# Kernel tuning notes

Measured on AMD Instinct MI355X. Metric: run time of the kernel, lower is better.

The kernel has to match this reference:

```python
import jax, jax.numpy as jnp
import numpy as np

N_TOTAL = 2_000_000   # total particles across all events
N_EVENTS = 20_000     # number of events (segments)
H = 64                # phi/rho hidden width
OUT = 10              # output classes


def _lin(x, W, b):
    # torch nn.Linear: y = x @ W.T + b
    return x @ W.T + b


def setup_inputs() -> dict:
    key = jax.random.key(0)
    ks = jax.random.split(key, 24)
    s = 0.1  # small init scale
    inp = {
        "values": jax.random.normal(ks[0], (N_TOTAL,), dtype=jnp.float32),
        "seg_ids": jnp.sort(jax.random.randint(ks[1], (N_TOTAL,), 0, N_EVENTS)),
        "p1w0": jax.random.normal(ks[2], (H, 1), dtype=jnp.float32) * s,
        "p1b0": jax.random.normal(ks[3], (H,), dtype=jnp.float32) * s,
        "p1w1": jax.random.normal(ks[4], (H, H), dtype=jnp.float32) * s,
        "p1b1": jax.random.normal(ks[5], (H,), dtype=jnp.float32) * s,
        "r1w0": jax.random.normal(ks[6], (H, H), dtype=jnp.float32) * s,
        "r1b0": jax.random.normal(ks[7], (H,), dtype=jnp.float32) * s,
        "r1w1": jax.random.normal(ks[8], (H, H), dtype=jnp.float32) * s,
        "r1b1": jax.random.normal(ks[9], (H,), dtype=jnp.float32) * s,
        "o1w": jax.random.normal(ks[10], (H, H), dtype=jnp.float32) * s,
        "o1b": jax.random.normal(ks[11], (H,), dtype=jnp.float32) * s,
        "p2w0": jax.random.normal(ks[12], (H, H), dtype=jnp.float32) * s,
        "p2b0": jax.random.normal(ks[13], (H,), dtype=jnp.float32) * s,
        "p2w1": jax.random.normal(ks[14], (H, H), dtype=jnp.float32) * s,
        "p2b1": jax.random.normal(ks[15], (H,), dtype=jnp.float32) * s,
        "r2w0": jax.random.normal(ks[16], (H, H), dtype=jnp.float32) * s,
        "r2b0": jax.random.normal(ks[17], (H,), dtype=jnp.float32) * s,
        "r2w1": jax.random.normal(ks[18], (H, H), dtype=jnp.float32) * s,
        "r2b1": jax.random.normal(ks[19], (H,), dtype=jnp.float32) * s,
        "o2w": jax.random.normal(ks[20], (OUT, H), dtype=jnp.float32) * s,
        "o2b": jax.random.normal(ks[21], (OUT,), dtype=jnp.float32) * s,
    }
    return inp


def reference(values, seg_ids, p1w0, p1b0, p1w1, p1b1, r1w0, r1b0, r1w1, r1b1,
              o1w, o1b, p2w0, p2b0, p2w1, p2b1, r2w0, r2b0, r2w1, r2b1, o2w, o2b):
    relu = jax.nn.relu
    # stage 1: phi1 on each scalar particle value -> [N, H]
    h = relu(_lin(values[:, None], p1w0, p1b0))
    h = relu(_lin(h, p1w1, p1b1))
    # jagged sum over particles within each event (the inner deepset sum)
    ev = jax.ops.segment_sum(h, seg_ids, num_segments=N_EVENTS)  # [E, H]
    # rho1 + output linear + activation per event
    ev = relu(_lin(ev, r1w0, r1b0))
    ev = relu(_lin(ev, r1w1, r1b1))
    ev = relu(_lin(ev, o1w, o1b))  # [E, H] (output_size of deepset1 = rho_sizes[-1])
    # stage 2: phi2 per event, sum over all events
    h2 = relu(_lin(ev, p2w0, p2b0))
    h2 = relu(_lin(h2, p2w1, p2b1))
    s2 = jnp.sum(h2, axis=0, keepdims=True)  # [1, H]
    r2 = relu(_lin(s2, r2w0, r2b0))
    r2 = relu(_lin(r2, r2w1, r2b1))
    out = _lin(r2, o2w, o2b)  # [1, OUT]
    return jax.nn.log_softmax(out, axis=1)
```

## Files before the change

### kernel.cpp

```cpp
#include <hip/hip_runtime.h>

#define NT 2000000
#define NE 20000
#define NTILES (NT / 64)
#define K1_BLOCKS 1024
#define K1_WAVES (K1_BLOCKS * 4)
#define TILES_BASE (NTILES / K1_WAVES)
#define TILES_REM (NTILES - TILES_BASE * K1_WAVES)
#define STAGE_CAP 24

using bf16x8 = __attribute__((ext_vector_type(8))) __bf16;
using half8  = __attribute__((ext_vector_type(8))) _Float16;
using half2v = __attribute__((ext_vector_type(2))) _Float16;
using f32x4  = __attribute__((ext_vector_type(4))) float;
using f32x2  = __attribute__((ext_vector_type(2))) float;
using fvec4  = __attribute__((ext_vector_type(4))) float;

__device__ __forceinline__ void load_bsplit(const float* __restrict__ p,
                                            bf16x8& hi, bf16x8& lo) {
    fvec4 a = *(const fvec4*)p;
    fvec4 b = *(const fvec4*)(p + 4);
#pragma unroll
    for (int e = 0; e < 4; e++) {
        float v  = a[e];
        __bf16 h = (__bf16)v;
        hi[e]    = h;
        lo[e]    = (__bf16)(v - (float)h);
        float v2  = b[e];
        __bf16 h2 = (__bf16)v2;
        hi[e + 4] = h2;
        lo[e + 4] = (__bf16)(v2 - (float)h2);
    }
}

__device__ __forceinline__ half8 load_h8(const float* __restrict__ p) {
    fvec4 a = *(const fvec4*)p;
    fvec4 b = *(const fvec4*)(p + 4);
    half8 r;
#pragma unroll
    for (int e = 0; e < 4; e++) {
        r[e]     = (_Float16)a[e];
        r[e + 4] = (_Float16)b[e];
    }
    return r;
}

__global__ __launch_bounds__(256, 4) void k1_phi1(
    const float* __restrict__ values, const int* __restrict__ seg,
    const float* __restrict__ w0, const float* __restrict__ b0,
    const float* __restrict__ w1, const float* __restrict__ b1,
    float* __restrict__ ev,
    float* __restrict__ stage, int* __restrict__ sid_arr,
    int* __restrict__ cnt_arr, int use_stage) {
    const int tid = threadIdx.x;
    const int w   = tid >> 6;
    const int l   = tid & 63;
    const int l15 = l & 15;
    const int l4  = l >> 4;

    half8 Bh[2][4];
#pragma unroll
    for (int kf = 0; kf < 2; kf++)
#pragma unroll
        for (int jf = 0; jf < 4; jf++)
            Bh[kf][jf] = load_h8(w1 + (jf * 16 + l15) * 64 + kf * 32 + l4 * 8);

    half2v w0h[2][4], b0h[2][4];
#pragma unroll
    for (int kf = 0; kf < 2; kf++) {
        const int kb = kf * 32 + l4 * 8;
#pragma unroll
        for (int e2 = 0; e2 < 4; e2++) {
            f32x2 wp = *(const f32x2*)(w0 + kb + 2 * e2);
            f32x2 bp = *(const f32x2*)(b0 + kb + 2 * e2);
            w0h[kf][e2] = half2v{(_Float16)wp[0], (_Float16)wp[1]};
            b0h[kf][e2] = half2v{(_Float16)bp[0], (_Float16)bp[1]};
        }
    }
    f32x4 biasC[4];
#pragma unroll
    for (int jf = 0; jf < 4; jf++) {
        const float bj = b1[jf * 16 + l15];
#pragma unroll
        for (int r = 0; r < 4; r++) biasC[jf][r] = bj;
    }

    const bool bit0 = (l & 16) != 0;
    const bool bit1 = (l & 32) != 0;
    auto reduce4 = [&](const float sj[4]) -> float {
        float send01 = bit0 ? sj[0] : sj[1];
        float keep01 = bit0 ? sj[1] : sj[0];
        float c01 = keep01 + __shfl_xor(send01, 16);
        float send23 = bit0 ? sj[2] : sj[3];
        float keep23 = bit0 ? sj[3] : sj[2];
        float c23 = keep23 + __shfl_xor(send23, 16);
        float send = bit1 ? c01 : c23;
        float keep = bit1 ? c23 : c01;
        return keep + __shfl_xor(send, 32);
    };

    const int wid   = blockIdx.x * 4 + w;
    const int start = wid * TILES_BASE + (wid < TILES_REM ? wid : TILES_REM);
    const int end   = start + TILES_BASE + (wid < TILES_REM ? 1 : 0);

    int nf = 0;
    auto FLUSH = [&](int sid, float* sj) {
        const float v = reduce4(sj);
        if (use_stage && nf < STAGE_CAP) {
            const int slot = wid * STAGE_CAP + nf;
            stage[(size_t)slot * 64 + l] = v;
            if (l == 0) sid_arr[slot] = sid;
            nf++;
        } else {
            atomicAdd(ev + (size_t)sid * 64 + l, v);
        }
    };

    int t = start;
    int s_cur = seg[t * 64 + l];
    half2v vph[2];
#pragma unroll
    for (int b = 0; b < 4; b++)
        vph[b >> 1][b & 1] = (_Float16)values[t * 64 + b * 16 + l15];

    int   cur = __builtin_amdgcn_readlane(s_cur, 0);
    float sj[4] = {0.f, 0.f, 0.f, 0.f};

    while (t < end) {
        const int nt = t + 1;
        int s_nxt = 0;
        half2v vpn[2];
#pragma unroll
        for (int i = 0; i < 2; i++) vpn[i] = half2v{(_Float16)0.f, (_Float16)0.f};
        if (nt < end) {
            s_nxt = seg[nt * 64 + l];
#pragma unroll
            for (int b = 0; b < 4; b++)
                vpn[b >> 1][b & 1] = (_Float16)values[nt * 64 + b * 16 + l15];
        }

        const int prev = __shfl_up(s_cur, 1);
        const bool diff = (l == 0) ? (s_cur != cur) : (s_cur != prev);
        const unsigned long long mask = __ballot(diff);

#pragma unroll
        for (int b = 0; b < 4; b++) {
            const unsigned mask16 = (unsigned)((mask >> (16 * b)) & 0xFFFFull);
            const _Float16 vh = vph[b >> 1][b & 1];
            const half2v vv = {vh, vh};

            half8 A0, A1;
#pragma unroll
            for (int e2 = 0; e2 < 4; e2++) {
                half2v h0 = vv * w0h[0][e2] + b0h[0][e2];
                half2v h1 = vv * w0h[1][e2] + b0h[1][e2];
                const _Float16 z = (_Float16)0.f;
                A0[2 * e2]     = h0[0] > z ? h0[0] : z;
                A0[2 * e2 + 1] = h0[1] > z ? h0[1] : z;
                A1[2 * e2]     = h1[0] > z ? h1[0] : z;
                A1[2 * e2 + 1] = h1[1] > z ? h1[1] : z;
            }

            f32x4 frag[4];
#pragma unroll
            for (int jf = 0; jf < 4; jf++) {
                f32x4 tt = __builtin_amdgcn_mfma_f32_16x16x32_f16(
                    A0, Bh[0][jf], biasC[jf], 0, 0, 0);
                tt = __builtin_amdgcn_mfma_f32_16x16x32_f16(
                    A1, Bh[1][jf], tt, 0, 0, 0);
#pragma unroll
                for (int r = 0; r < 4; r++) frag[jf][r] = fmaxf(tt[r], 0.f);
            }

            if (mask16 == 0u) {
#pragma unroll
                for (int jf = 0; jf < 4; jf++)
                    sj[jf] += (frag[jf][0] + frag[jf][1]) +
                              (frag[jf][2] + frag[jf][3]);
            } else {
                unsigned m = mask16;
                int st = 0;
                while (true) {
                    const int e = m ? (int)__builtin_ctz(m) : 16;
#pragma unroll
                    for (int jf = 0; jf < 4; jf++) {
                        float s = 0.f;
#pragma unroll
                        for (int r = 0; r < 4; r++) {
                            const int rel = l4 * 4 + r;
                            s += (rel >= st && rel < e) ? frag[jf][r] : 0.f;
                        }
                        sj[jf] += s;
                    }
                    if (!m) break;
                    FLUSH(cur, sj);
                    sj[0] = sj[1] = sj[2] = sj[3] = 0.f;
                    cur = __builtin_amdgcn_readlane(s_cur, 16 * b + e);
                    st  = e;
                    m &= (m - 1);
                }
            }
        }

        t = nt;
        s_cur = s_nxt;
        vph[0] = vpn[0];
        vph[1] = vpn[1];
    }
    FLUSH(cur, sj);
    if (use_stage && l == 0) cnt_arr[wid] = nf;
}

__global__ __launch_bounds__(256) void k1_combine(
    const float* __restrict__ stage, const int* __restrict__ sid_arr,
    const int* __restrict__ cnt_arr, float* __restrict__ ev) {
    const int w = threadIdx.x >> 6, l = threadIdx.x & 63;
    const int wid = blockIdx.x * 4 + w;
    const int n = cnt_arr[wid];
    for (int c = 0; c < n; ++c) {
        const int slot = wid * STAGE_CAP + c;
        const int sid  = sid_arr[slot];
        atomicAdd(ev + (size_t)sid * 64 + l, stage[(size_t)slot * 64 + l]);
    }
}

__global__ __launch_bounds__(64) void k2_events(
    const float* __restrict__ ev,
    const float* __restrict__ W0, const float* __restrict__ B0,
    const float* __restrict__ W1, const float* __restrict__ B1,
    const float* __restrict__ W2, const float* __restrict__ B2,
    const float* __restrict__ W3, const float* __restrict__ B3,
    const float* __restrict__ W4, const float* __restrict__ B4,
    float* __restrict__ s2) {
    __shared__ __align__(16) __bf16 xt[64 * 72];
    const int l   = threadIdx.x;
    const int l15 = l & 15;
    const int l4  = l >> 4;
    const int ebase = blockIdx.x * 64;

    const float* Ws[5] = {W0, W1, W2, W3, W4};
    const float* Bs[5] = {B0, B1, B2, B3, B4};

    bf16x8 A[4][2];
#pragma unroll
    for (int pf = 0; pf < 4; pf++) {
        const int e = ebase + pf * 16 + l15;
#pragma unroll
        for (int kf = 0; kf < 2; kf++) {
            bf16x8 a;
            if (e < NE) {
                const float* p = ev + (size_t)e * 64 + kf * 32 + l4 * 8;
                fvec4 x = *(const fvec4*)p;
                fvec4 y = *(const fvec4*)(p + 4);
#pragma unroll
                for (int e2 = 0; e2 < 4; e2++) {
                    a[e2]     = (__bf16)x[e2];
                    a[e2 + 4] = (__bf16)y[e2];
                }
            } else {
#pragma unroll
                for (int e2 = 0; e2 < 8; e2++) a[e2] = (__bf16)0.f;
            }
            A[pf][kf] = a;
        }
    }

#pragma unroll
    for (int L = 0; L < 5; L++) {
        bf16x8 Bh[2][4], Bl[2][4];
#pragma unroll
        for (int kf = 0; kf < 2; kf++)
#pragma unroll
            for (int jf = 0; jf < 4; jf++)
                load_bsplit(Ws[L] + (jf * 16 + l15) * 64 + kf * 32 + l4 * 8,
                            Bh[kf][jf], Bl[kf][jf]);

        f32x4 acc[4][4];
#pragma unroll
        for (int jf = 0; jf < 4; jf++) {
            const float bj = Bs[L][jf * 16 + l15];
#pragma unroll
            for (int pf = 0; pf < 4; pf++)
#pragma unroll
                for (int r = 0; r < 4; r++) acc[pf][jf][r] = bj;
        }
#pragma unroll
        for (int kf = 0; kf < 2; kf++)
#pragma unroll
            for (int pf = 0; pf < 4; pf++)
#pragma unroll
                for (int jf = 0; jf < 4; jf++)
                    acc[pf][jf] = __builtin_amdgcn_mfma_f32_16x16x32_bf16(
                        A[pf][kf], Bh[kf][jf], acc[pf][jf], 0, 0, 0);
#pragma unroll
        for (int kf = 0; kf < 2; kf++)
#pragma unroll
            for (int pf = 0; pf < 4; pf++)
#pragma unroll
                for (int jf = 0; jf < 4; jf++)
                    acc[pf][jf] = __builtin_amdgcn_mfma_f32_16x16x32_bf16(
                        A[pf][kf], Bl[kf][jf], acc[pf][jf], 0, 0, 0);

        if (L < 4) {
#pragma unroll
            for (int pf = 0; pf < 4; pf++)
#pragma unroll
                for (int jf = 0; jf < 4; jf++) {
                    const int j = jf * 16 + l15;
#pragma unroll
                    for (int r = 0; r < 4; r++)
                        xt[(pf * 16 + l4 * 4 + r) * 72 + j] =
                            (__bf16)fmaxf(acc[pf][jf][r], 0.f);
                }
#pragma unroll
            for (int pf = 0; pf < 4; pf++)
#pragma unroll
                for (int kf = 0; kf < 2; kf++)
                    A[pf][kf] = *(const bf16x8*)(xt + (pf * 16 + l15) * 72 +
                                                 kf * 32 + l4 * 8);
        } else {
            float sj[4];
#pragma unroll
            for (int jf = 0; jf < 4; jf++) {
                float s = 0.f;
#pragma unroll
                for (int pf = 0; pf < 4; pf++)
#pragma unroll
                    for (int r = 0; r < 4; r++) {
                        const int e = ebase + pf * 16 + l4 * 4 + r;
                        float v = fmaxf(acc[pf][jf][r], 0.f);
                        s += (e < NE) ? v : 0.f;
                    }
                s += __shfl_xor(s, 16);
                s += __shfl_xor(s, 32);
                sj[jf] = s;
            }
            float v = (l4 == 0) ? sj[0] : (l4 == 1) ? sj[1]
                    : (l4 == 2) ? sj[2] : sj[3];
            atomicAdd(s2 + l, v);
        }
    }
}

__global__ __launch_bounds__(64) void k3_final(
    const float* __restrict__ s2,
    const float* __restrict__ W0, const float* __restrict__ B0,
    const float* __restrict__ W1, const float* __restrict__ B1,
    const float* __restrict__ W2, const float* __restrict__ B2,
    float* __restrict__ out) {
    __shared__ __align__(16) float xb[64];
    __shared__ __align__(16) float yb[64];
    __shared__ float ob[10];
    const int l = threadIdx.x;

    xb[l] = s2[l];
    __syncthreads();

    float a = B0[l];
#pragma unroll
    for (int k = 0; k < 16; k++) {
        fvec4 wv = *(const fvec4*)(W0 + l * 64 + k * 4);
        fvec4 xv = *(const fvec4*)(xb + k * 4);
        a += wv[0] * xv[0] + wv[1] * xv[1] + wv[2] * xv[2] + wv[3] * xv[3];
    }
    yb[l] = fmaxf(a, 0.f);
    __syncthreads();

    float b_ = B1[l];
#pragma unroll
    for (int k = 0; k < 16; k++) {
        fvec4 wv = *(const fvec4*)(W1 + l * 64 + k * 4);
        fvec4 xv = *(const fvec4*)(yb + k * 4);
        b_ += wv[0] * xv[0] + wv[1] * xv[1] + wv[2] * xv[2] + wv[3] * xv[3];
    }
    __syncthreads();
    xb[l] = fmaxf(b_, 0.f);
    __syncthreads();

    if (l < 10) {
        float o = B2[l];
#pragma unroll
        for (int k = 0; k < 16; k++) {
            fvec4 wv = *(const fvec4*)(W2 + l * 64 + k * 4);
            fvec4 xv = *(const fvec4*)(xb + k * 4);
            o += wv[0] * xv[0] + wv[1] * xv[1] + wv[2] * xv[2] + wv[3] * xv[3];
        }
        ob[l] = o;
    }
    __syncthreads();
    if (l == 0) {
        float m = ob[0];
#pragma unroll
        for (int i = 1; i < 10; i++) m = fmaxf(m, ob[i]);
        float sum = 0.f;
#pragma unroll
        for (int i = 0; i < 10; i++) sum = sum + expf(ob[i] - m);
        float ls = logf(sum);
#pragma unroll
        for (int i = 0; i < 10; i++) out[i] = ob[i] - m - ls;
    }
}

extern "C" void kernel_launch(void* const* d_in, const int* in_sizes, int n_in,
                              void* d_out, int out_size, void* d_ws, size_t ws_size,
                              hipStream_t stream) {
    const float* values = (const float*)d_in[0];
    const int*   seg    = (const int*)d_in[1];
    const float* p1w0 = (const float*)d_in[2],  *p1b0 = (const float*)d_in[3];
    const float* p1w1 = (const float*)d_in[4],  *p1b1 = (const float*)d_in[5];
    const float* r1w0 = (const float*)d_in[6],  *r1b0 = (const float*)d_in[7];
    const float* r1w1 = (const float*)d_in[8],  *r1b1 = (const float*)d_in[9];
    const float* o1w  = (const float*)d_in[10], *o1b  = (const float*)d_in[11];
    const float* p2w0 = (const float*)d_in[12], *p2b0 = (const float*)d_in[13];
    const float* p2w1 = (const float*)d_in[14], *p2b1 = (const float*)d_in[15];
    const float* r2w0 = (const float*)d_in[16], *r2b0 = (const float*)d_in[17];
    const float* r2w1 = (const float*)d_in[18], *r2b1 = (const float*)d_in[19];
    const float* o2w  = (const float*)d_in[20], *o2b  = (const float*)d_in[21];

    float* ev = (float*)d_ws;
    float* s2 = ev + (size_t)NE * 64;
    int*   cnt_arr = (int*)(s2 + 64);
    int*   sid_arr = cnt_arr + K1_WAVES;
    float* stage   = (float*)(sid_arr + (size_t)K1_WAVES * STAGE_CAP);

    const size_t need = ((size_t)NE * 64 + 64) * 4 +
                        (size_t)K1_WAVES * 4 +
                        (size_t)K1_WAVES * STAGE_CAP * 4 +
                        (size_t)K1_WAVES * STAGE_CAP * 64 * 4;
    const int use_stage = (ws_size >= need) ? 1 : 0;

    hipMemsetAsync(d_ws, 0, (size_t)(NE * 64 + 64) * sizeof(float), stream);

    hipLaunchKernelGGL(k1_phi1, dim3(K1_BLOCKS), dim3(256), 0, stream,
                       values, seg, p1w0, p1b0, p1w1, p1b1, ev,
                       stage, sid_arr, cnt_arr, use_stage);
    if (use_stage) {
        hipLaunchKernelGGL(k1_combine, dim3(K1_WAVES / 4), dim3(256), 0, stream,
                           stage, sid_arr, cnt_arr, ev);
    }
    hipLaunchKernelGGL(k2_events, dim3((NE + 63) / 64), dim3(64), 0, stream,
                       ev, r1w0, r1b0, r1w1, r1b1, o1w, o1b,
                       p2w0, p2b0, p2w1, p2b1, s2);
    hipLaunchKernelGGL(k3_final, dim3(1), dim3(64), 0, stream,
                       s2, r2w0, r2b0, r2w1, r2b1, o2w, o2b, (float*)d_out);
}
```

Measured before the change: 73.00 us.

## Compute segment offsets and assign whole events per wave without atomics

```diff
diff --git a/kernel.cpp b/kernel.cpp
--- a/kernel.cpp
+++ b/kernel.cpp
@@ -2,12 +2,8 @@
 
 #define NT 2000000
 #define NE 20000
-#define NTILES (NT / 64)
-#define K1_BLOCKS 1024
-#define K1_WAVES (K1_BLOCKS * 4)
-#define TILES_BASE (NTILES / K1_WAVES)
-#define TILES_REM (NTILES - TILES_BASE * K1_WAVES)
-#define STAGE_CAP 24
+#define NT4 (NT / 4)
+#define EPW 5
 
 using bf16x8 = __attribute__((ext_vector_type(8))) __bf16;
 using half8  = __attribute__((ext_vector_type(8))) _Float16;
@@ -45,13 +41,33 @@
     return r;
 }
 
+__global__ __launch_bounds__(256) void k0_offsets(
+    const int* __restrict__ seg, int* __restrict__ off, float* __restrict__ s2) {
+    if (blockIdx.x == 0 && threadIdx.x < 64) s2[threadIdx.x] = 0.f;
+    const int g = blockIdx.x * 256 + threadIdx.x;
+    if (g >= NT4) return;
+    const int idx4 = g * 4;
+    const int4 s = *(const int4*)(seg + idx4);
+    int prev = (g == 0) ? -1 : seg[idx4 - 1];
+    int vals[4] = {s.x, s.y, s.z, s.w};
+#pragma unroll
+    for (int k = 0; k < 4; k++) {
+        const int cur = vals[k];
+        if (cur != prev) {
+            for (int e = prev + 1; e <= cur; ++e) off[e] = idx4 + k;
+        }
+        prev = cur;
+    }
+    if (idx4 + 3 == NT - 1) {
+        for (int e = prev + 1; e <= NE; ++e) off[e] = NT;
+    }
+}
+
 __global__ __launch_bounds__(256, 4) void k1_phi1(
-    const float* __restrict__ values, const int* __restrict__ seg,
+    const float* __restrict__ values, const int* __restrict__ off,
     const float* __restrict__ w0, const float* __restrict__ b0,
     const float* __restrict__ w1, const float* __restrict__ b1,
-    float* __restrict__ ev,
-    float* __restrict__ stage, int* __restrict__ sid_arr,
-    int* __restrict__ cnt_arr, int use_stage) {
+    float* __restrict__ ev) {
     const int tid = threadIdx.x;
     const int w   = tid >> 6;
     const int l   = tid & 63;
@@ -99,128 +115,68 @@
         return keep + __shfl_xor(send, 32);
     };
 
-    const int wid   = blockIdx.x * 4 + w;
-    const int start = wid * TILES_BASE + (wid < TILES_REM ? wid : TILES_REM);
-    const int end   = start + TILES_BASE + (wid < TILES_REM ? 1 : 0);
-
-    int nf = 0;
-    auto FLUSH = [&](int sid, float* sj) {
-        const float v = reduce4(sj);
-        if (use_stage && nf < STAGE_CAP) {
-            const int slot = wid * STAGE_CAP + nf;
-            stage[(size_t)slot * 64 + l] = v;
-            if (l == 0) sid_arr[slot] = sid;
-            nf++;
-        } else {
-            atomicAdd(ev + (size_t)sid * 64 + l, v);
-        }
-    };
-
-    int t = start;
-    int s_cur = seg[t * 64 + l];
-    half2v vph[2];
-#pragma unroll
-    for (int b = 0; b < 4; b++)
-        vph[b >> 1][b & 1] = (_Float16)values[t * 64 + b * 16 + l15];
-
-    int   cur = __builtin_amdgcn_readlane(s_cur, 0);
-    float sj[4] = {0.f, 0.f, 0.f, 0.f};
-
-    while (t < end) {
-        const int nt = t + 1;
-        int s_nxt = 0;
-        half2v vpn[2];
-#pragma unroll
-        for (int i = 0; i < 2; i++) vpn[i] = half2v{(_Float16)0.f, (_Float16)0.f};
-        if (nt < end) {
-            s_nxt = seg[nt * 64 + l];
-#pragma unroll
-            for (int b = 0; b < 4; b++)
-                vpn[b >> 1][b & 1] = (_Float16)values[nt * 64 + b * 16 + l15];
-        }
-
-        const int prev = __shfl_up(s_cur, 1);
-        const bool diff = (l == 0) ? (s_cur != cur) : (s_cur != prev);
-        const unsigned long long mask = __ballot(diff);
-
-#pragma unroll
-        for (int b = 0; b < 4; b++) {
-            const unsigned mask16 = (unsigned)((mask >> (16 * b)) & 0xFFFFull);
-            const _Float16 vh = vph[b >> 1][b & 1];
-            const half2v vv = {vh, vh};
-
-            half8 A0, A1;
-#pragma unroll
-            for (int e2 = 0; e2 < 4; e2++) {
-                half2v h0 = vv * w0h[0][e2] + b0h[0][e2];
-                half2v h1 = vv * w0h[1][e2] + b0h[1][e2];
-                const _Float16 z = (_Float16)0.f;
-                A0[2 * e2]     = h0[0] > z ? h0[0] : z;
-                A0[2 * e2 + 1] = h0[1] > z ? h0[1] : z;
-                A1[2 * e2]     = h1[0] > z ? h1[0] : z;
-                A1[2 * e2 + 1] = h1[1] > z ? h1[1] : z;
+    const int wid = blockIdx.x * 4 + w;
+    const int e0  = wid * EPW;
+
+    for (int e = e0; e < e0 + EPW && e < NE; ++e) {
+        const int s = off[e];
+        const int t = off[e + 1];
+        const int n = t - s;
+        float sj[4] = {0.f, 0.f, 0.f, 0.f};
+
+        if (n > 0) {
+            const int nblk = (n + 15) >> 4;
+            int idx = s + l15;
+            _Float16 vcur = (_Float16)((idx < t) ? values[idx] : 0.f);
+
+            for (int b = 0; b < nblk; ++b) {
+                const int idxn = s + (b + 1) * 16 + l15;
+                const _Float16 vnxt =
+                    (_Float16)((b + 1 < nblk && idxn < t) ? values[idxn] : 0.f);
+
+                const half2v vv = {vcur, vcur};
+                half8 A0, A1;
+#pragma unroll
+                for (int e2 = 0; e2 < 4; e2++) {
+                    half2v h0 = vv * w0h[0][e2] + b0h[0][e2];
+                    half2v h1 = vv * w0h[1][e2] + b0h[1][e2];
+                    const _Float16 z = (_Float16)0.f;
+                    A0[2 * e2]     = h0[0] > z ? h0[0] : z;
+                    A0[2 * e2 + 1] = h0[1] > z ? h0[1] : z;
+                    A1[2 * e2]     = h1[0] > z ? h1[0] : z;
+                    A1[2 * e2 + 1] = h1[1] > z ? h1[1] : z;
+                }
+
+                f32x4 frag[4];
+#pragma unroll
+                for (int jf = 0; jf < 4; jf++) {
+                    f32x4 tt = __builtin_amdgcn_mfma_f32_16x16x32_f16(
+                        A0, Bh[0][jf], biasC[jf], 0, 0, 0);
+                    tt = __builtin_amdgcn_mfma_f32_16x16x32_f16(
+                        A1, Bh[1][jf], tt, 0, 0, 0);
+#pragma unroll
+                    for (int r = 0; r < 4; r++) frag[jf][r] = fmaxf(tt[r], 0.f);
+                }
+
+                const int rem = n - b * 16;
+                if (rem >= 16) {
+#pragma unroll
+                    for (int jf = 0; jf < 4; jf++)
+                        sj[jf] += (frag[jf][0] + frag[jf][1]) +
+                                  (frag[jf][2] + frag[jf][3]);
+                } else {
+#pragma unroll
+                    for (int r = 0; r < 4; r++) {
+                        const bool ok = (l4 * 4 + r) < rem;
+#pragma unroll
+                        for (int jf = 0; jf < 4; jf++)
+                            sj[jf] += ok ? frag[jf][r] : 0.f;
+                    }
+                }
+                vcur = vnxt;
             }
-
-            f32x4 frag[4];
-#pragma unroll
-            for (int jf = 0; jf < 4; jf++) {
-                f32x4 tt = __builtin_amdgcn_mfma_f32_16x16x32_f16(
-                    A0, Bh[0][jf], biasC[jf], 0, 0, 0);
-                tt = __builtin_amdgcn_mfma_f32_16x16x32_f16(
-                    A1, Bh[1][jf], tt, 0, 0, 0);
-#pragma unroll
-                for (int r = 0; r < 4; r++) frag[jf][r] = fmaxf(tt[r], 0.f);
-            }
-
-            if (mask16 == 0u) {
-#pragma unroll
-                for (int jf = 0; jf < 4; jf++)
-                    sj[jf] += (frag[jf][0] + frag[jf][1]) +
-                              (frag[jf][2] + frag[jf][3]);
-            } else {
-                unsigned m = mask16;
-                int st = 0;
-                while (true) {
-                    const int e = m ? (int)__builtin_ctz(m) : 16;
-#pragma unroll
-                    for (int jf = 0; jf < 4; jf++) {
-                        float s = 0.f;
-#pragma unroll
-                        for (int r = 0; r < 4; r++) {
-                            const int rel = l4 * 4 + r;
-                            s += (rel >= st && rel < e) ? frag[jf][r] : 0.f;
-                        }
-                        sj[jf] += s;
-                    }
-                    if (!m) break;
-                    FLUSH(cur, sj);
-                    sj[0] = sj[1] = sj[2] = sj[3] = 0.f;
-                    cur = __builtin_amdgcn_readlane(s_cur, 16 * b + e);
-                    st  = e;
-                    m &= (m - 1);
-                }
-            }
-        }
-
-        t = nt;
-        s_cur = s_nxt;
-        vph[0] = vpn[0];
-        vph[1] = vpn[1];
-    }
-    FLUSH(cur, sj);
-    if (use_stage && l == 0) cnt_arr[wid] = nf;
-}
-
-__global__ __launch_bounds__(256) void k1_combine(
-    const float* __restrict__ stage, const int* __restrict__ sid_arr,
-    const int* __restrict__ cnt_arr, float* __restrict__ ev) {
-    const int w = threadIdx.x >> 6, l = threadIdx.x & 63;
-    const int wid = blockIdx.x * 4 + w;
-    const int n = cnt_arr[wid];
-    for (int c = 0; c < n; ++c) {
-        const int slot = wid * STAGE_CAP + c;
-        const int sid  = sid_arr[slot];
-        atomicAdd(ev + (size_t)sid * 64 + l, stage[(size_t)slot * 64 + l]);
+        }
+        ev[(size_t)e * 64 + l] = reduce4(sj);
     }
 }
 
@@ -417,27 +373,14 @@
     const float* r2w1 = (const float*)d_in[18], *r2b1 = (const float*)d_in[19];
     const float* o2w  = (const float*)d_in[20], *o2b  = (const float*)d_in[21];
 
-    float* ev = (float*)d_ws;
-    float* s2 = ev + (size_t)NE * 64;
-    int*   cnt_arr = (int*)(s2 + 64);
-    int*   sid_arr = cnt_arr + K1_WAVES;
-    float* stage   = (float*)(sid_arr + (size_t)K1_WAVES * STAGE_CAP);
-
-    const size_t need = ((size_t)NE * 64 + 64) * 4 +
-                        (size_t)K1_WAVES * 4 +
-                        (size_t)K1_WAVES * STAGE_CAP * 4 +
-                        (size_t)K1_WAVES * STAGE_CAP * 64 * 4;
-    const int use_stage = (ws_size >= need) ? 1 : 0;
-
-    hipMemsetAsync(d_ws, 0, (size_t)(NE * 64 + 64) * sizeof(float), stream);
-
-    hipLaunchKernelGGL(k1_phi1, dim3(K1_BLOCKS), dim3(256), 0, stream,
-                       values, seg, p1w0, p1b0, p1w1, p1b1, ev,
-                       stage, sid_arr, cnt_arr, use_stage);
-    if (use_stage) {
-        hipLaunchKernelGGL(k1_combine, dim3(K1_WAVES / 4), dim3(256), 0, stream,
-                           stage, sid_arr, cnt_arr, ev);
-    }
+    float* ev  = (float*)d_ws;
+    float* s2  = ev + (size_t)NE * 64;
+    int*   off = (int*)(s2 + 64);
+
+    hipLaunchKernelGGL(k0_offsets, dim3((NT4 + 255) / 256), dim3(256), 0, stream,
+                       seg, off, s2);
+    hipLaunchKernelGGL(k1_phi1, dim3(1024), dim3(256), 0, stream,
+                       values, off, p1w0, p1b0, p1w1, p1b1, ev);
     hipLaunchKernelGGL(k2_events, dim3((NE + 63) / 64), dim3(64), 0, stream,
                        ev, r1w0, r1b0, r1w1, r1b1, o1w, o1b,
                        p2w0, p2b0, p2w1, p2b1, s2);
```

Measured after the change: 71.87 us. No clear change (-1.5%).
